# Performance work log

Hardware: AMD Instinct MI355X
Metric: run time of the kernel (lower is better)

## Reference

```python
import jax, jax.numpy as jnp
import numpy as np

EMBED_DIM = 1024
NUM_HEADS = 16
HEAD_DIM = EMBED_DIM // NUM_HEADS
BATCH = 2
SEQ = 2048


def setup_inputs() -> dict:
    key = jax.random.key(0)
    ks = jax.random.split(key, 9)
    s = 1.0 / np.sqrt(EMBED_DIM)
    x = jax.random.normal(ks[0], (BATCH, SEQ, EMBED_DIM), dtype=jnp.float32)
    Wq = jax.random.uniform(ks[1], (EMBED_DIM, EMBED_DIM), jnp.float32, -s, s)
    bq = jax.random.uniform(ks[2], (EMBED_DIM,), jnp.float32, -s, s)
    Wk = jax.random.uniform(ks[3], (EMBED_DIM, EMBED_DIM), jnp.float32, -s, s)
    bk = jax.random.uniform(ks[4], (EMBED_DIM,), jnp.float32, -s, s)
    Wv = jax.random.uniform(ks[5], (EMBED_DIM, EMBED_DIM), jnp.float32, -s, s)
    bv = jax.random.uniform(ks[6], (EMBED_DIM,), jnp.float32, -s, s)
    Wo = jax.random.uniform(ks[7], (EMBED_DIM, EMBED_DIM), jnp.float32, -s, s)
    bo = jax.random.uniform(ks[8], (EMBED_DIM,), jnp.float32, -s, s)
    return {"x": x, "Wq": Wq, "bq": bq, "Wk": Wk, "bk": bk,
            "Wv": Wv, "bv": bv, "Wo": Wo, "bo": bo}


def reference(x, Wq, bq, Wk, bk, Wv, bv, Wo, bo):
    B, S, E = x.shape
    H, D = NUM_HEADS, HEAD_DIM

    def split_heads(t):
        # [B, S, E] -> [B, H, S, D]
        return t.reshape(B, S, H, D).transpose(0, 2, 1, 3)

    q = split_heads(x @ Wq + bq)
    k = split_heads(x @ Wk + bk)
    v = split_heads(x @ Wv + bv)

    scale = 1.0 / np.sqrt(D).astype(np.float32)
    scores = jnp.einsum('bhqd,bhkd->bhqk', q, k) * scale  # [B,H,S,S]
    attn = jax.nn.softmax(scores, axis=-1)
    out = jnp.einsum('bhqk,bhkd->bhqd', attn, v)  # [B,H,S,D]
    out = out.transpose(0, 2, 1, 3).reshape(B, S, E)
    return out @ Wo + bo
```

## Files before the change

### kernel.cpp

```cpp
#include <hip/hip_runtime.h>
#include <cstdint>

#define BATCH 2
#define SEQ   2048
#define EMB   1024
#define NHEAD 16
#define HDIM  64
#define NTOK  (BATCH*SEQ)

typedef __attribute__((ext_vector_type(8))) short bf16x8;
typedef __attribute__((ext_vector_type(8))) short short8;
typedef __attribute__((ext_vector_type(4))) float f32x4;

__device__ inline unsigned short f2bf(float f) {
    unsigned u = __float_as_uint(f);
    u += 0x7FFF + ((u >> 16) & 1);
    return (unsigned short)(u >> 16);
}

__device__ inline unsigned cvt_pk_bf16(float lo, float hi) {
    unsigned r;
    asm("v_cvt_pk_bf16_f32 %0, %1, %2" : "=v"(r) : "v"(lo), "v"(hi));
    return r;
}

__device__ inline void gload16(const void* g, void* lds) {
    __builtin_amdgcn_global_load_lds(
        (const __attribute__((address_space(1))) unsigned int*)g,
        (__attribute__((address_space(3))) unsigned int*)lds, 16, 0, 0);
}

__global__ __launch_bounds__(256)
void conv_x(const float* __restrict__ x, unsigned short* __restrict__ xb) {
    int i = (blockIdx.x * 256 + threadIdx.x) * 8;
    float4 a = *(const float4*)(x + i);
    float4 b = *(const float4*)(x + i + 4);
    short8 o;
    o[0]=f2bf(a.x); o[1]=f2bf(a.y); o[2]=f2bf(a.z); o[3]=f2bf(a.w);
    o[4]=f2bf(b.x); o[5]=f2bf(b.y); o[6]=f2bf(b.z); o[7]=f2bf(b.w);
    *(short8*)(xb + i) = o;
}

__global__ __launch_bounds__(256)
void conv_wt(const float* __restrict__ Wq, const float* __restrict__ Wk,
             const float* __restrict__ Wv, const float* __restrict__ Wo,
             unsigned short* __restrict__ Wt) {
    const float* W = blockIdx.z==0?Wq : blockIdx.z==1?Wk : blockIdx.z==2?Wv : Wo;
    unsigned short* out = Wt + (size_t)blockIdx.z * EMB * EMB;
    __shared__ float T[64][68];
    const int t = threadIdx.x;
    const int k0 = blockIdx.x * 64, n0 = blockIdx.y * 64;
    #pragma unroll
    for (int rr = 0; rr < 4; ++rr) {
        int row = (t >> 4) + 16 * rr;
        float4 v = *(const float4*)(W + (size_t)(k0+row)*EMB + n0 + (t&15)*4);
        *(float4*)&T[row][(t&15)*4] = v;
    }
    __syncthreads();
    #pragma unroll
    for (int it = 0; it < 2; ++it) {
        int ci = it*256 + t;
        int nr = ci >> 3, kc = ci & 7;
        short8 o;
        #pragma unroll
        for (int j = 0; j < 8; ++j) o[j] = f2bf(T[kc*8+j][nr]);
        *(short8*)(out + (size_t)(n0+nr)*EMB + k0 + kc*8) = o;
    }
}

__global__ __launch_bounds__(256)
void transpose_v(const unsigned short* __restrict__ Vb, unsigned short* __restrict__ Vt) {
    __shared__ unsigned short T[64*65];
    const int t = threadIdx.x;
    const int s0 = blockIdx.x * 64;
    const int bh = blockIdx.y;
    const int b = bh >> 4, h = bh & 15;
    const unsigned short* src = Vb + ((size_t)b*SEQ + s0)*EMB + h*HDIM;
    #pragma unroll
    for (int it = 0; it < 2; ++it) {
        int ci = it*256 + t;
        int r = ci >> 3, c = ci & 7;
        short8 v = *(const short8*)(src + (size_t)r*EMB + c*8);
        #pragma unroll
        for (int j = 0; j < 8; ++j) T[r*65 + c*8 + j] = (unsigned short)v[j];
    }
    __syncthreads();
    unsigned short* dst = Vt + (size_t)bh * HDIM * SEQ + s0;
    #pragma unroll
    for (int it = 0; it < 2; ++it) {
        int ci = it*256 + t;
        int d = ci >> 3, c = ci & 7;
        short8 o;
        #pragma unroll
        for (int j = 0; j < 8; ++j) o[j] = (short)T[(c*8 + j)*65 + d];
        *(short8*)(dst + (size_t)d*SEQ + c*8) = o;
    }
}

__global__ __launch_bounds__(256)
void gemm_qkv(const unsigned short* __restrict__ xb, const unsigned short* __restrict__ Wt,
              const float* __restrict__ bq, const float* __restrict__ bk,
              const float* __restrict__ bv,
              unsigned short* __restrict__ Qb, unsigned short* __restrict__ Kb,
              unsigned short* __restrict__ Vb) {
    const int z = blockIdx.z;
    const unsigned short* W = Wt + (size_t)z * EMB * EMB;
    const float* bias = z==0 ? bq : z==1 ? bk : bv;
    unsigned short* out = z==0 ? Qb : z==1 ? Kb : Vb;
    const float scale = z==0 ? (0.125f * 1.44269504f) : 1.0f;

    __shared__ __align__(16) unsigned short As[2][128*32];
    __shared__ __align__(16) unsigned short Bs[2][128*32];

    const int tid = threadIdx.x, lane = tid & 63, wid = tid >> 6;
    const int m0 = blockIdx.y * 128, n0 = blockIdx.x * 128;
    const int wr = wid >> 1, wc = wid & 1;

    const int ci0 = tid, ci1 = 256 + tid;
    const int row0 = ci0 >> 2, c0 = (ci0 & 3) ^ ((row0 >> 1) & 3);
    const int row1 = ci1 >> 2, c1 = (ci1 & 3) ^ ((row1 >> 1) & 3);
    const int dst0 = wid*64, dst1 = 256 + wid*64;

    f32x4 acc[4][4];
    #pragma unroll
    for (int i = 0; i < 4; ++i)
        #pragma unroll
        for (int j = 0; j < 4; ++j) acc[i][j] = f32x4{0.f,0.f,0.f,0.f};

    gload16(xb + (size_t)(m0+row0)*EMB + c0*8, (char*)As[0] + dst0*16);
    gload16(W  + (size_t)(n0+row0)*EMB + c0*8, (char*)Bs[0] + dst0*16);
    gload16(xb + (size_t)(m0+row1)*EMB + c1*8, (char*)As[0] + dst1*16);
    gload16(W  + (size_t)(n0+row1)*EMB + c1*8, (char*)Bs[0] + dst1*16);
    __syncthreads();

    for (int kk = 0; kk < EMB/32; ++kk) {
        const int cur = kk & 1;
        if (kk < EMB/32 - 1) {
            int k0 = (kk+1) * 32;
            gload16(xb + (size_t)(m0+row0)*EMB + k0 + c0*8, (char*)As[cur^1] + dst0*16);
            gload16(W  + (size_t)(n0+row0)*EMB + k0 + c0*8, (char*)Bs[cur^1] + dst0*16);
            gload16(xb + (size_t)(m0+row1)*EMB + k0 + c1*8, (char*)As[cur^1] + dst1*16);
            gload16(W  + (size_t)(n0+row1)*EMB + k0 + c1*8, (char*)Bs[cur^1] + dst1*16);
        }
        bf16x8 af[4], bf[4];
        #pragma unroll
        for (int i = 0; i < 4; ++i) {
            int ar = 64*wr + 16*i + (lane & 15);
            int ac = (lane >> 4) ^ ((ar >> 1) & 3);
            af[i] = *(const bf16x8*)((const char*)As[cur] + ar*64 + ac*16);
            int br = 64*wc + 16*i + (lane & 15);
            int bc = (lane >> 4) ^ ((br >> 1) & 3);
            bf[i] = *(const bf16x8*)((const char*)Bs[cur] + br*64 + bc*16);
        }
        __builtin_amdgcn_s_setprio(1);
        #pragma unroll
        for (int i = 0; i < 4; ++i)
            #pragma unroll
            for (int j = 0; j < 4; ++j)
                acc[i][j] = __builtin_amdgcn_mfma_f32_16x16x32_bf16(af[i], bf[j], acc[i][j], 0, 0, 0);
        __builtin_amdgcn_s_setprio(0);
        __syncthreads();
    }

    #pragma unroll
    for (int j = 0; j < 4; ++j) {
        int col = n0 + 64*wc + 16*j + (lane & 15);
        float bvv = bias[col];
        #pragma unroll
        for (int i = 0; i < 4; ++i) {
            int rw0 = m0 + 64*wr + 16*i + (lane >> 4) * 4;
            #pragma unroll
            for (int r = 0; r < 4; ++r)
                out[(size_t)(rw0+r)*EMB + col] = f2bf((acc[i][j][r] + bvv) * scale);
        }
    }
}

__global__ __launch_bounds__(256)
void gemm_out(const unsigned short* __restrict__ Cb, const unsigned short* __restrict__ Wto,
              const float* __restrict__ bo, float* __restrict__ out) {
    __shared__ __align__(16) unsigned short As[2][64*32];
    __shared__ __align__(16) unsigned short Bs[2][128*32];

    const int tid = threadIdx.x, lane = tid & 63, wid = tid >> 6;
    const int m0 = blockIdx.y * 64, n0 = blockIdx.x * 128;
    const int wr = wid >> 1, wc = wid & 1;

    const int arow_ = tid >> 2, ac_ = (tid & 3) ^ ((arow_ >> 1) & 3);
    const int ci1 = 256 + tid;
    const int brow0 = tid >> 2, bc0 = (tid & 3) ^ ((brow0 >> 1) & 3);
    const int brow1 = ci1 >> 2, bc1 = (ci1 & 3) ^ ((brow1 >> 1) & 3);
    const int dst0 = wid*64, dst1 = 256 + wid*64;

    f32x4 acc[2][4];
    #pragma unroll
    for (int i = 0; i < 2; ++i)
        #pragma unroll
        for (int j = 0; j < 4; ++j) acc[i][j] = f32x4{0.f,0.f,0.f,0.f};

    gload16(Cb  + (size_t)(m0+arow_)*EMB + ac_*8, (char*)As[0] + dst0*16);
    gload16(Wto + (size_t)(n0+brow0)*EMB + bc0*8, (char*)Bs[0] + dst0*16);
    gload16(Wto + (size_t)(n0+brow1)*EMB + bc1*8, (char*)Bs[0] + dst1*16);
    __syncthreads();

    for (int kk = 0; kk < EMB/32; ++kk) {
        const int cur = kk & 1;
        if (kk < EMB/32 - 1) {
            int k0 = (kk+1) * 32;
            gload16(Cb  + (size_t)(m0+arow_)*EMB + k0 + ac_*8, (char*)As[cur^1] + dst0*16);
            gload16(Wto + (size_t)(n0+brow0)*EMB + k0 + bc0*8, (char*)Bs[cur^1] + dst0*16);
            gload16(Wto + (size_t)(n0+brow1)*EMB + k0 + bc1*8, (char*)Bs[cur^1] + dst1*16);
        }
        bf16x8 af[2], bf[4];
        #pragma unroll
        for (int i = 0; i < 2; ++i) {
            int ar = 32*wr + 16*i + (lane & 15);
            int ac = (lane >> 4) ^ ((ar >> 1) & 3);
            af[i] = *(const bf16x8*)((const char*)As[cur] + ar*64 + ac*16);
        }
        #pragma unroll
        for (int j = 0; j < 4; ++j) {
            int br = 64*wc + 16*j + (lane & 15);
            int bc = (lane >> 4) ^ ((br >> 1) & 3);
            bf[j] = *(const bf16x8*)((const char*)Bs[cur] + br*64 + bc*16);
        }
        __builtin_amdgcn_s_setprio(1);
        #pragma unroll
        for (int i = 0; i < 2; ++i)
            #pragma unroll
            for (int j = 0; j < 4; ++j)
                acc[i][j] = __builtin_amdgcn_mfma_f32_16x16x32_bf16(af[i], bf[j], acc[i][j], 0, 0, 0);
        __builtin_amdgcn_s_setprio(0);
        __syncthreads();
    }

    #pragma unroll
    for (int j = 0; j < 4; ++j) {
        int col = n0 + 64*wc + 16*j + (lane & 15);
        float bvv = bo[col];
        #pragma unroll
        for (int i = 0; i < 2; ++i) {
            int row0 = m0 + 32*wr + 16*i + (lane >> 4) * 4;
            #pragma unroll
            for (int r = 0; r < 4; ++r)
                out[(size_t)(row0+r)*EMB + col] = acc[i][j][r] + bvv;
        }
    }
}

__global__ __launch_bounds__(256, 4)
void attn(const unsigned short* __restrict__ Qg, const unsigned short* __restrict__ Kg,
          const unsigned short* __restrict__ Vt, unsigned short* __restrict__ Cg) {
    __shared__ __align__(16) unsigned short Ks[2][64*64];
    __shared__ __align__(16) unsigned short Vs[2][64*64];

    const int tid = threadIdx.x, lane = tid & 63, wid = tid >> 6;
    const int qb = blockIdx.x, bh = blockIdx.y;
    const int b = bh >> 4, h = bh & 15;
    const size_t base = (size_t)b * SEQ * EMB + (size_t)h * HDIM;
    const unsigned short* Qp = Qg + base + (size_t)qb * 64 * EMB;
    const unsigned short* Kp = Kg + base;
    const unsigned short* Vtp = Vt + (size_t)bh * HDIM * SEQ;

    #pragma unroll
    for (int it = 0; it < 2; ++it) {
        int ci = it*256 + tid, row = ci >> 3, c = (ci & 7) ^ (row & 7);
        gload16(Qp + (size_t)row*EMB + c*8, (char*)Ks[0] + (it*256 + wid*64)*16);
    }
    __syncthreads();
    bf16x8 qf[2];
    #pragma unroll
    for (int kc = 0; kc < 2; ++kc) {
        int r = 16*wid + (lane & 15);
        int c = ((lane >> 4) + 4*kc) ^ (r & 7);
        qf[kc] = *(const bf16x8*)((const char*)Ks[0] + r*128 + c*16);
    }
    __syncthreads();

    #pragma unroll
    for (int it = 0; it < 2; ++it) {
        int ci = it*256 + tid, row = ci >> 3, c = (ci & 7) ^ (row & 7);
        gload16(Kp + (size_t)row*EMB + c*8, (char*)Ks[0] + (it*256 + wid*64)*16);
        gload16(Vtp + (size_t)row*SEQ + c*8, (char*)Vs[0] + (it*256 + wid*64)*16);
    }
    __syncthreads();

    f32x4 O[4];
    #pragma unroll
    for (int j = 0; j < 4; ++j) O[j] = f32x4{0.f,0.f,0.f,0.f};
    float l_run = 0.f;

    for (int kt = 0; kt < SEQ/64; ++kt) {
        const int cur = kt & 1, nxt = cur ^ 1;
        if (kt < SEQ/64 - 1) {
            const unsigned short* Kt = Kp + (size_t)(kt+1)*64*EMB;
            const unsigned short* Vn = Vtp + (size_t)(kt+1)*64;
            #pragma unroll
            for (int it = 0; it < 2; ++it) {
                int ci = it*256 + tid, row = ci >> 3, c = (ci & 7) ^ (row & 7);
                gload16(Kt + (size_t)row*EMB + c*8, (char*)Ks[nxt] + (it*256 + wid*64)*16);
                gload16(Vn + (size_t)row*SEQ + c*8, (char*)Vs[nxt] + (it*256 + wid*64)*16);
            }
        }

        f32x4 s[4];
        __builtin_amdgcn_s_setprio(1);
        #pragma unroll
        for (int nk = 0; nk < 4; ++nk) {
            s[nk] = f32x4{0.f,0.f,0.f,0.f};
            #pragma unroll
            for (int kc = 0; kc < 2; ++kc) {
                int r = 16*nk + (lane & 15);
                int c = ((lane >> 4) + 4*kc) ^ (r & 7);
                bf16x8 kf = *(const bf16x8*)((const char*)Ks[cur] + r*128 + c*16);
                s[nk] = __builtin_amdgcn_mfma_f32_16x16x32_bf16(kf, qf[kc], s[nk], 0, 0, 0);
            }
        }
        __builtin_amdgcn_s_setprio(0);

        float psv[4];
        #pragma unroll
        for (int nk = 0; nk < 4; ++nk) {
            #pragma unroll
            for (int r = 0; r < 4; ++r)
                s[nk][r] = exp2f(s[nk][r]);
            psv[nk] = (s[nk][0] + s[nk][1]) + (s[nk][2] + s[nk][3]);
        }
        float ps = (psv[0] + psv[1]) + (psv[2] + psv[3]);
        ps += __shfl_xor(ps, 16);
        ps += __shfl_xor(ps, 32);
        l_run += ps;

        unsigned pk[4][2];
        #pragma unroll
        for (int nk = 0; nk < 4; ++nk) {
            pk[nk][0] = cvt_pk_bf16(s[nk][0], s[nk][1]);
            pk[nk][1] = cvt_pk_bf16(s[nk][2], s[nk][3]);
        }
        const int hh = lane >> 4;
        const int srcA = (((hh << 1) & 3) << 4) | (lane & 15);
        const int srcB = srcA + 16;
        const int hs = hh >> 1;
        bf16x8 pf[2];
        #pragma unroll
        for (int kc = 0; kc < 2; ++kc) {
            union { unsigned u[4]; bf16x8 v; } cvt;
            unsigned a0 = __shfl((int)pk[2*kc][0], srcA), b0 = __shfl((int)pk[2*kc+1][0], srcA);
            cvt.u[0] = hs ? b0 : a0;
            unsigned a1 = __shfl((int)pk[2*kc][1], srcA), b1 = __shfl((int)pk[2*kc+1][1], srcA);
            cvt.u[1] = hs ? b1 : a1;
            unsigned a2 = __shfl((int)pk[2*kc][0], srcB), b2 = __shfl((int)pk[2*kc+1][0], srcB);
            cvt.u[2] = hs ? b2 : a2;
            unsigned a3 = __shfl((int)pk[2*kc][1], srcB), b3 = __shfl((int)pk[2*kc+1][1], srcB);
            cvt.u[3] = hs ? b3 : a3;
            pf[kc] = cvt.v;
        }

        __builtin_amdgcn_s_setprio(1);
        #pragma unroll
        for (int jd = 0; jd < 4; ++jd) {
            #pragma unroll
            for (int kc = 0; kc < 2; ++kc) {
                int d = 16*jd + (lane & 15);
                int c = ((lane >> 4) + 4*kc) ^ (d & 7);
                bf16x8 vf = *(const bf16x8*)((const char*)Vs[cur] + d*128 + c*16);
                O[jd] = __builtin_amdgcn_mfma_f32_16x16x32_bf16(pf[kc], vf, O[jd], 0, 0, 0);
            }
        }
        __builtin_amdgcn_s_setprio(0);
        __syncthreads();
    }

    float inv[4];
    #pragma unroll
    for (int r = 0; r < 4; ++r) inv[r] = 1.f / __shfl(l_run, (lane >> 4)*4 + r);
    unsigned short* Cp = Cg + base + (size_t)qb * 64 * EMB;
    #pragma unroll
    for (int jd = 0; jd < 4; ++jd)
        #pragma unroll
        for (int r = 0; r < 4; ++r) {
            int row = 16*wid + (lane >> 4)*4 + r;
            int col = 16*jd + (lane & 15);
            Cp[(size_t)row*EMB + col] = f2bf(O[jd][r] * inv[r]);
        }
}

extern "C" void kernel_launch(void* const* d_in, const int* in_sizes, int n_in,
                              void* d_out, int out_size, void* d_ws, size_t ws_size,
                              hipStream_t stream) {
    const float* x  = (const float*)d_in[0];
    const float* Wq = (const float*)d_in[1];
    const float* bq = (const float*)d_in[2];
    const float* Wk = (const float*)d_in[3];
    const float* bk = (const float*)d_in[4];
    const float* Wv = (const float*)d_in[5];
    const float* bv = (const float*)d_in[6];
    const float* Wo = (const float*)d_in[7];
    const float* bo = (const float*)d_in[8];
    float* out = (float*)d_out;

    unsigned short* xb = (unsigned short*)d_ws;
    unsigned short* Wt = xb + (size_t)NTOK * EMB;
    unsigned short* Qb = Wt + (size_t)4 * EMB * EMB;
    unsigned short* Kb = Qb + (size_t)NTOK * EMB;
    unsigned short* Vb = Kb + (size_t)NTOK * EMB;
    unsigned short* Cb = Vb + (size_t)NTOK * EMB;
    unsigned short* Vtr = Cb + (size_t)NTOK * EMB;

    conv_x<<<dim3((NTOK*EMB)/(256*8)), 256, 0, stream>>>(x, xb);
    conv_wt<<<dim3(16, 16, 4), 256, 0, stream>>>(Wq, Wk, Wv, Wo, Wt);
    gemm_qkv<<<dim3(8, 32, 3), 256, 0, stream>>>(xb, Wt, bq, bk, bv, Qb, Kb, Vb);
    transpose_v<<<dim3(SEQ/64, BATCH*NHEAD), 256, 0, stream>>>(Vb, Vtr);
    attn<<<dim3(SEQ/64, BATCH*NHEAD), 256, 0, stream>>>(Qb, Kb, Vtr, Cb);
    gemm_out<<<dim3(EMB/128, NTOK/64), 256, 0, stream>>>(Cb, Wt + (size_t)3*EMB*EMB, bo, out);
}
```

Baseline: 219.9 us.

## Retile QKV GEMM to 256x256 blocks with BK=64 over concatenated weights

```diff
diff --git a/kernel.cpp b/kernel.cpp
--- a/kernel.cpp
+++ b/kernel.cpp
@@ -97,81 +97,91 @@
     }
 }
 
-__global__ __launch_bounds__(256)
+__global__ __launch_bounds__(512, 2)
 void gemm_qkv(const unsigned short* __restrict__ xb, const unsigned short* __restrict__ Wt,
               const float* __restrict__ bq, const float* __restrict__ bk,
               const float* __restrict__ bv,
               unsigned short* __restrict__ Qb, unsigned short* __restrict__ Kb,
               unsigned short* __restrict__ Vb) {
-    const int z = blockIdx.z;
-    const unsigned short* W = Wt + (size_t)z * EMB * EMB;
-    const float* bias = z==0 ? bq : z==1 ? bk : bv;
-    unsigned short* out = z==0 ? Qb : z==1 ? Kb : Vb;
-    const float scale = z==0 ? (0.125f * 1.44269504f) : 1.0f;
-
-    __shared__ __align__(16) unsigned short As[2][128*32];
-    __shared__ __align__(16) unsigned short Bs[2][128*32];
+    __shared__ __align__(16) unsigned short As[2][256*64];
+    __shared__ __align__(16) unsigned short Bs[2][256*64];
 
     const int tid = threadIdx.x, lane = tid & 63, wid = tid >> 6;
-    const int m0 = blockIdx.y * 128, n0 = blockIdx.x * 128;
-    const int wr = wid >> 1, wc = wid & 1;
-
-    const int ci0 = tid, ci1 = 256 + tid;
-    const int row0 = ci0 >> 2, c0 = (ci0 & 3) ^ ((row0 >> 1) & 3);
-    const int row1 = ci1 >> 2, c1 = (ci1 & 3) ^ ((row1 >> 1) & 3);
-    const int dst0 = wid*64, dst1 = 256 + wid*64;
-
-    f32x4 acc[4][4];
-    #pragma unroll
-    for (int i = 0; i < 4; ++i)
+    const int m0 = blockIdx.y * 256, n0 = blockIdx.x * 256;
+    const int wr = wid >> 2, wc = wid & 3;
+
+    f32x4 acc[8][4];
+    #pragma unroll
+    for (int i = 0; i < 8; ++i)
         #pragma unroll
         for (int j = 0; j < 4; ++j) acc[i][j] = f32x4{0.f,0.f,0.f,0.f};
 
-    gload16(xb + (size_t)(m0+row0)*EMB + c0*8, (char*)As[0] + dst0*16);
-    gload16(W  + (size_t)(n0+row0)*EMB + c0*8, (char*)Bs[0] + dst0*16);
-    gload16(xb + (size_t)(m0+row1)*EMB + c1*8, (char*)As[0] + dst1*16);
-    gload16(W  + (size_t)(n0+row1)*EMB + c1*8, (char*)Bs[0] + dst1*16);
-    __syncthreads();
-
-    for (int kk = 0; kk < EMB/32; ++kk) {
+    int srow[4], sc[4], sdst[4];
+    #pragma unroll
+    for (int it = 0; it < 4; ++it) {
+        int ci = it*512 + tid;
+        srow[it] = ci >> 3;
+        sc[it]   = (ci & 7) ^ (srow[it] & 7);
+        sdst[it] = (it*512 + wid*64) * 16;
+    }
+
+    #pragma unroll
+    for (int it = 0; it < 4; ++it) {
+        gload16(xb + (size_t)(m0+srow[it])*EMB + sc[it]*8, (char*)As[0] + sdst[it]);
+        gload16(Wt + (size_t)(n0+srow[it])*EMB + sc[it]*8, (char*)Bs[0] + sdst[it]);
+    }
+    __syncthreads();
+
+    for (int kk = 0; kk < EMB/64; ++kk) {
         const int cur = kk & 1;
-        if (kk < EMB/32 - 1) {
-            int k0 = (kk+1) * 32;
-            gload16(xb + (size_t)(m0+row0)*EMB + k0 + c0*8, (char*)As[cur^1] + dst0*16);
-            gload16(W  + (size_t)(n0+row0)*EMB + k0 + c0*8, (char*)Bs[cur^1] + dst0*16);
-            gload16(xb + (size_t)(m0+row1)*EMB + k0 + c1*8, (char*)As[cur^1] + dst1*16);
-            gload16(W  + (size_t)(n0+row1)*EMB + k0 + c1*8, (char*)Bs[cur^1] + dst1*16);
-        }
-        bf16x8 af[4], bf[4];
-        #pragma unroll
-        for (int i = 0; i < 4; ++i) {
-            int ar = 64*wr + 16*i + (lane & 15);
-            int ac = (lane >> 4) ^ ((ar >> 1) & 3);
-            af[i] = *(const bf16x8*)((const char*)As[cur] + ar*64 + ac*16);
-            int br = 64*wc + 16*i + (lane & 15);
-            int bc = (lane >> 4) ^ ((br >> 1) & 3);
-            bf[i] = *(const bf16x8*)((const char*)Bs[cur] + br*64 + bc*16);
-        }
-        __builtin_amdgcn_s_setprio(1);
-        #pragma unroll
-        for (int i = 0; i < 4; ++i)
-            #pragma unroll
-            for (int j = 0; j < 4; ++j)
-                acc[i][j] = __builtin_amdgcn_mfma_f32_16x16x32_bf16(af[i], bf[j], acc[i][j], 0, 0, 0);
-        __builtin_amdgcn_s_setprio(0);
+        if (kk < EMB/64 - 1) {
+            int k0 = (kk+1) * 64;
+            #pragma unroll
+            for (int it = 0; it < 4; ++it) {
+                gload16(xb + (size_t)(m0+srow[it])*EMB + k0 + sc[it]*8, (char*)As[cur^1] + sdst[it]);
+                gload16(Wt + (size_t)(n0+srow[it])*EMB + k0 + sc[it]*8, (char*)Bs[cur^1] + sdst[it]);
+            }
+        }
+        #pragma unroll
+        for (int kc = 0; kc < 2; ++kc) {
+            bf16x8 af[8], bf[4];
+            #pragma unroll
+            for (int i = 0; i < 8; ++i) {
+                int r = 128*wr + 16*i + (lane & 15);
+                int c = ((lane >> 4) + 4*kc) ^ (r & 7);
+                af[i] = *(const bf16x8*)((const char*)As[cur] + r*128 + c*16);
+            }
+            #pragma unroll
+            for (int j = 0; j < 4; ++j) {
+                int r = 64*wc + 16*j + (lane & 15);
+                int c = ((lane >> 4) + 4*kc) ^ (r & 7);
+                bf[j] = *(const bf16x8*)((const char*)Bs[cur] + r*128 + c*16);
+            }
+            #pragma unroll
+            for (int i = 0; i < 8; ++i)
+                #pragma unroll
+                for (int j = 0; j < 4; ++j)
+                    acc[i][j] = __builtin_amdgcn_mfma_f32_16x16x32_bf16(af[i], bf[j], acc[i][j], 0, 0, 0);
+        }
         __syncthreads();
     }
 
+    const int zsel = n0 >> 10;
+    const float* bias = zsel==0 ? bq : zsel==1 ? bk : bv;
+    unsigned short* out = zsel==0 ? Qb : zsel==1 ? Kb : Vb;
+    const int nL = n0 & 1023;
+    const float scale = zsel==0 ? (0.125f * 1.44269504f) : 1.0f;
+
     #pragma unroll
     for (int j = 0; j < 4; ++j) {
-        int col = n0 + 64*wc + 16*j + (lane & 15);
-        float bvv = bias[col];
-        #pragma unroll
-        for (int i = 0; i < 4; ++i) {
-            int rw0 = m0 + 64*wr + 16*i + (lane >> 4) * 4;
+        int colL = nL + 64*wc + 16*j + (lane & 15);
+        float bvv = bias[colL];
+        #pragma unroll
+        for (int i = 0; i < 8; ++i) {
+            int row0 = m0 + 128*wr + 16*i + (lane >> 4) * 4;
             #pragma unroll
             for (int r = 0; r < 4; ++r)
-                out[(size_t)(rw0+r)*EMB + col] = f2bf((acc[i][j][r] + bvv) * scale);
+                out[(size_t)(row0+r)*EMB + colL] = f2bf((acc[i][j][r] + bvv) * scale);
         }
     }
 }
@@ -224,13 +234,11 @@
             int bc = (lane >> 4) ^ ((br >> 1) & 3);
             bf[j] = *(const bf16x8*)((const char*)Bs[cur] + br*64 + bc*16);
         }
-        __builtin_amdgcn_s_setprio(1);
         #pragma unroll
         for (int i = 0; i < 2; ++i)
             #pragma unroll
             for (int j = 0; j < 4; ++j)
                 acc[i][j] = __builtin_amdgcn_mfma_f32_16x16x32_bf16(af[i], bf[j], acc[i][j], 0, 0, 0);
-        __builtin_amdgcn_s_setprio(0);
         __syncthreads();
     }
 
@@ -409,7 +417,7 @@
 
     conv_x<<<dim3((NTOK*EMB)/(256*8)), 256, 0, stream>>>(x, xb);
     conv_wt<<<dim3(16, 16, 4), 256, 0, stream>>>(Wq, Wk, Wv, Wo, Wt);
-    gemm_qkv<<<dim3(8, 32, 3), 256, 0, stream>>>(xb, Wt, bq, bk, bv, Qb, Kb, Vb);
+    gemm_qkv<<<dim3(12, 16), 512, 0, stream>>>(xb, Wt, bq, bk, bv, Qb, Kb, Vb);
     transpose_v<<<dim3(SEQ/64, BATCH*NHEAD), 256, 0, stream>>>(Vb, Vtr);
     attn<<<dim3(SEQ/64, BATCH*NHEAD), 256, 0, stream>>>(Qb, Kb, Vtr, Cb);
     gemm_out<<<dim3(EMB/128, NTOK/64), 256, 0, stream>>>(Cb, Wt + (size_t)3*EMB*EMB, bo, out);
```

Result: slower. 225.3 us (+2.5%).
